# Optimization experiments

Measured on AMD Instinct MI355X. Metric: run time of the kernel, lower is better.

The kernel has to match this reference:

```python
import jax, jax.numpy as jnp
import numpy as np

D_MODEL, D_STATE, D_CONV, EXPAND = 1024, 16, 4, 2
D_INNER = D_MODEL * EXPAND


def setup_inputs() -> dict:
    key = jax.random.key(0)
    ks = jax.random.split(key, 12)
    s = lambda fan_in: 1.0 / np.sqrt(fan_in)
    return {
        "x": jax.random.normal(ks[0], (2, 2048, D_MODEL), dtype=jnp.float32),
        "W_in": jax.random.normal(ks[1], (D_MODEL, 2 * D_INNER), dtype=jnp.float32) * s(D_MODEL),
        "b_in": jnp.zeros((2 * D_INNER,), jnp.float32),
        "W_conv": jax.random.normal(ks[2], (D_INNER, 1, D_CONV), dtype=jnp.float32) * s(D_CONV),
        "b_conv": jnp.zeros((D_INNER,), jnp.float32),
        "A_log": jax.random.normal(ks[3], (D_INNER, D_STATE), dtype=jnp.float32) * -0.5 - 1.0,
        "D": jnp.ones((D_INNER,), jnp.float32),
        "W_B": jax.random.normal(ks[4], (D_INNER, D_STATE), dtype=jnp.float32) * s(D_INNER),
        "b_B": jnp.zeros((D_STATE,), jnp.float32),
        "W_C": jax.random.normal(ks[5], (D_INNER, D_STATE), dtype=jnp.float32) * s(D_INNER),
        "b_C": jnp.zeros((D_STATE,), jnp.float32),
        "W_out": jax.random.normal(ks[6], (D_INNER, D_MODEL), dtype=jnp.float32) * s(D_INNER),
        "b_out": jnp.zeros((D_MODEL,), jnp.float32),
    }


def reference(x, W_in, b_in, W_conv, b_conv, A_log, D, W_B, b_B, W_C, b_C, W_out, b_out):
    B, L, _ = x.shape
    xz = x @ W_in + b_in                       # (B, L, 2*D_INNER)
    xi, z = jnp.split(xz, 2, axis=-1)
    # depthwise causal conv1d (left pad d_conv-1, truncate to L)
    xc = jnp.swapaxes(xi, 1, 2)                # (B, D_INNER, L)
    xc = jax.lax.conv_general_dilated(
        xc, W_conv, window_strides=(1,), padding=[(D_CONV - 1, 0)],
        dimension_numbers=("NCH", "OIH", "NCH"), feature_group_count=D_INNER)
    xc = xc + b_conv[None, :, None]
    xi = jnp.swapaxes(xc, 1, 2)                # (B, L, D_INNER)
    xi = jax.nn.silu(xi)

    A = -jnp.exp(jnp.clip(A_log, -10.0, 2.0))  # (D_INNER, D_STATE)
    Bm = xi @ W_B + b_B                        # (B, L, D_STATE)
    Cm = xi @ W_C + b_C                        # (B, L, D_STATE)

    def step(h, inp):
        x_t, B_t, C_t = inp                    # (B,D_INNER), (B,D_STATE), (B,D_STATE)
        h = h * A[None] + x_t[:, :, None] * B_t[:, None, :]
        h = jnp.clip(h, -100.0, 100.0)
        y = jnp.einsum("bds,bs->bd", h, C_t) + D * x_t
        y = jnp.clip(y, -100.0, 100.0)
        return h, y

    h0 = jnp.zeros((B, D_INNER, D_STATE), x.dtype)
    xs = (jnp.swapaxes(xi, 0, 1), jnp.swapaxes(Bm, 0, 1), jnp.swapaxes(Cm, 0, 1))
    _, ys = jax.lax.scan(step, h0, xs)         # ys: (L, B, D_INNER)
    y = jnp.swapaxes(ys, 0, 1)                 # (B, L, D_INNER)
    y = y * jax.nn.sigmoid(z)
    return y @ W_out + b_out
```

## Files before the change

kernel.cpp:

```cpp
#include <hip/hip_runtime.h>
#include <hip/hip_bf16.h>
#include <math.h>

#define B_SZ   2
#define L_SZ   2048
#define DM     1024
#define DI     2048
#define DS     16
#define M_SZ   (B_SZ * L_SZ)
#define N_XZ   (2 * DI)
#define LDF    20
#define SEGS   32
#define SEGLEN 64
#define SEG1   32
#define KZN    8

typedef short bf16x8 __attribute__((ext_vector_type(8)));
typedef float f32x4  __attribute__((ext_vector_type(4)));

__device__ __forceinline__ unsigned short rne16(float f) {
  unsigned int u = __builtin_bit_cast(unsigned int, f);
  u += 0x7FFFu + ((u >> 16) & 1u);
  return (unsigned short)(u >> 16);
}
__device__ __forceinline__ float frombf(unsigned short h) {
  unsigned int u = ((unsigned int)h) << 16;
  return __builtin_bit_cast(float, u);
}

__global__ __launch_bounds__(256) void convert_x(
    const float* __restrict__ x, unsigned short* __restrict__ xh,
    unsigned short* __restrict__ xl) {
  int i = (blockIdx.x * 256 + threadIdx.x) * 4;
  float4 v = *(const float4*)(x + i);
  unsigned short h0 = rne16(v.x), h1 = rne16(v.y), h2 = rne16(v.z), h3 = rne16(v.w);
  *(ushort4*)(xh + i) = make_ushort4(h0, h1, h2, h3);
  *(ushort4*)(xl + i) = make_ushort4(rne16(v.x - frombf(h0)), rne16(v.y - frombf(h1)),
                                     rne16(v.z - frombf(h2)), rne16(v.w - frombf(h3)));
}

__global__ __launch_bounds__(256) void transpose_w(
    const float* __restrict__ in, int R, int C,
    unsigned short* __restrict__ oh, unsigned short* __restrict__ ol) {
  __shared__ float T[64][65];
  const int tid = threadIdx.x;
  const int c0 = blockIdx.x * 64, r0 = blockIdx.y * 64;
  const int cc = tid & 63, rq = tid >> 6;
  #pragma unroll
  for (int i = 0; i < 16; ++i) {
    int r = rq * 16 + i;
    T[r][cc] = in[(size_t)(r0 + r) * C + c0 + cc];
  }
  __syncthreads();
  #pragma unroll
  for (int i = 0; i < 16; ++i) {
    int c = rq * 16 + i;
    float v = T[cc][c];
    size_t o = (size_t)(c0 + c) * R + r0 + cc;
    unsigned short h = rne16(v);
    oh[o] = h;
    if (ol) ol[o] = rne16(v - frombf(h));
  }
}

template<int BN, bool X3, bool OUTBF16>
__global__ __launch_bounds__(256, X3 ? 3 : 4) void gemm_t(
    const unsigned short* __restrict__ Ah, const unsigned short* __restrict__ Al, int lda,
    const unsigned short* __restrict__ Bh, const unsigned short* __restrict__ Bl, int ldb,
    const float* __restrict__ bias, float* __restrict__ Cf,
    unsigned short* __restrict__ Cz, int ldc, int K) {
  constexpr int WN  = BN / 2;
  constexpr int FJ  = BN / 32;
  constexpr int BCH = BN / 64;
  __shared__ unsigned int AhS[128 * LDF];
  __shared__ unsigned int BhS[BN * LDF];
  __shared__ unsigned int AlS[X3 ? 128 * LDF : 4];
  __shared__ unsigned int BlS[X3 ? BN * LDF : 4];
  const int tid  = threadIdx.x;
  const int lane = tid & 63, wave = tid >> 6;
  const int wr = wave >> 1, wc = wave & 1;
  const int lm = lane & 15, lq = lane >> 4;
  const int row0 = blockIdx.y * 128, col0 = blockIdx.x * BN;

  f32x4 acc[4][FJ];
  #pragma unroll
  for (int i = 0; i < 4; ++i)
    #pragma unroll
    for (int j = 0; j < FJ; ++j) acc[i][j] = (f32x4){0.f, 0.f, 0.f, 0.f};

  for (int k0 = 0; k0 < K; k0 += 32) {
    __syncthreads();
    #pragma unroll
    for (int i = 0; i < 2; ++i) {
      int idx = tid + i * 256, r = idx >> 2, q = idx & 3;
      size_t go = (size_t)(row0 + r) * lda + k0 + q * 8;
      *(uint4*)&AhS[r * LDF + q * 4] = *(const uint4*)(Ah + go);
      if constexpr (X3)
        *(uint4*)&AlS[r * LDF + q * 4] = *(const uint4*)(Al + go);
    }
    #pragma unroll
    for (int i = 0; i < BCH; ++i) {
      int idx = tid + i * 256, r = idx >> 2, q = idx & 3;
      size_t go = (size_t)(col0 + r) * ldb + k0 + q * 8;
      *(uint4*)&BhS[r * LDF + q * 4] = *(const uint4*)(Bh + go);
      if constexpr (X3)
        *(uint4*)&BlS[r * LDF + q * 4] = *(const uint4*)(Bl + go);
    }
    __syncthreads();
    bf16x8 bh[FJ], bl[FJ];
    #pragma unroll
    for (int j = 0; j < FJ; ++j) {
      bh[j] = *(const bf16x8*)&BhS[(wc * WN + j * 16 + lm) * LDF + lq * 4];
      if constexpr (X3)
        bl[j] = *(const bf16x8*)&BlS[(wc * WN + j * 16 + lm) * LDF + lq * 4];
    }
    #pragma unroll
    for (int i = 0; i < 4; ++i) {
      bf16x8 ah = *(const bf16x8*)&AhS[(wr * 64 + i * 16 + lm) * LDF + lq * 4];
      bf16x8 al;
      if constexpr (X3)
        al = *(const bf16x8*)&AlS[(wr * 64 + i * 16 + lm) * LDF + lq * 4];
      #pragma unroll
      for (int j = 0; j < FJ; ++j) {
        acc[i][j] = __builtin_amdgcn_mfma_f32_16x16x32_bf16(ah, bh[j], acc[i][j], 0, 0, 0);
        if constexpr (X3) {
          acc[i][j] = __builtin_amdgcn_mfma_f32_16x16x32_bf16(ah, bl[j], acc[i][j], 0, 0, 0);
          acc[i][j] = __builtin_amdgcn_mfma_f32_16x16x32_bf16(al, bh[j], acc[i][j], 0, 0, 0);
        }
      }
    }
  }
  #pragma unroll
  for (int i = 0; i < 4; ++i) {
    #pragma unroll
    for (int j = 0; j < FJ; ++j) {
      int c = col0 + wc * WN + j * 16 + lm;
      float bs = bias[c];
      #pragma unroll
      for (int k = 0; k < 4; ++k) {
        int r = row0 + wr * 64 + i * 16 + lq * 4 + k;
        float v = acc[i][j][k] + bs;
        if constexpr (OUTBF16) Cz[(size_t)r * ldc + c] = rne16(v);
        else                   Cf[(size_t)r * ldc + c] = v;
      }
    }
  }
}

__global__ __launch_bounds__(256) void conv_silu_kernel(
    const float* __restrict__ xi, const float* __restrict__ Wc,
    const float* __restrict__ bc, float* __restrict__ xc) {
  int idx = blockIdx.x * blockDim.x + threadIdx.x;
  if (idx >= M_SZ * DI) return;
  int d  = idx & (DI - 1);
  int bl = idx >> 11;
  int l  = bl & (L_SZ - 1);
  float4 w = ((const float4*)Wc)[d];
  const float* base = xi + (size_t)bl * DI + d;
  float s = bc[d] + base[0] * w.w;
  if (l >= 1) s = fmaf(base[-DI],     w.z, s);
  if (l >= 2) s = fmaf(base[-2 * DI], w.y, s);
  if (l >= 3) s = fmaf(base[-3 * DI], w.x, s);
  float sig = 1.f / (1.f + expf(-s));
  xc[idx] = s * sig;
}

__global__ __launch_bounds__(256) void prep_wbc(
    const float* __restrict__ WB, const float* __restrict__ WC,
    unsigned short* __restrict__ Wh, unsigned short* __restrict__ Wl) {
  int idx = blockIdx.x * 256 + threadIdx.x;
  int c = idx >> 11, k = idx & 2047;
  float v = 0.f;
  if (c < 32) {
    const float* W = (c & 1) ? WC : WB;
    v = W[k * DS + (c >> 1)];
  }
  unsigned short h = rne16(v);
  Wh[idx] = h;
  Wl[idx] = rne16(v - frombf(h));
}

__global__ __launch_bounds__(256, 3) void gemm_bcf(
    const float* __restrict__ Af, int lda,
    const unsigned short* __restrict__ Bh, const unsigned short* __restrict__ Bl, int ldb,
    float* __restrict__ parts, int ldc, int Kslice) {
  __shared__ unsigned int AhS[128 * LDF];
  __shared__ unsigned int AlS[128 * LDF];
  __shared__ unsigned int BhS[64 * LDF];
  __shared__ unsigned int BlS[64 * LDF];
  const int tid  = threadIdx.x;
  const int lane = tid & 63, wave = tid >> 6;
  const int wr = wave >> 1, wc = wave & 1;
  const int lm = lane & 15, lq = lane >> 4;
  const int row0 = blockIdx.y * 128;
  const int kbase = blockIdx.x * Kslice;
  float* Cp = parts + (size_t)blockIdx.x * M_SZ * 64;

  f32x4 acc[4][2];
  #pragma unroll
  for (int i = 0; i < 4; ++i)
    #pragma unroll
    for (int j = 0; j < 2; ++j) acc[i][j] = (f32x4){0.f, 0.f, 0.f, 0.f};

  for (int k0 = kbase; k0 < kbase + Kslice; k0 += 32) {
    __syncthreads();
    #pragma unroll
    for (int i = 0; i < 4; ++i) {
      int idx = tid + i * 256, r = idx >> 3, q = idx & 7;
      float4 v = *(const float4*)(Af + (size_t)(row0 + r) * lda + k0 + q * 4);
      unsigned short h0 = rne16(v.x), h1 = rne16(v.y), h2 = rne16(v.z), h3 = rne16(v.w);
      AhS[r * LDF + q * 2]     = (unsigned)h0 | ((unsigned)h1 << 16);
      AhS[r * LDF + q * 2 + 1] = (unsigned)h2 | ((unsigned)h3 << 16);
      unsigned short l0 = rne16(v.x - frombf(h0)), l1 = rne16(v.y - frombf(h1));
      unsigned short l2 = rne16(v.z - frombf(h2)), l3 = rne16(v.w - frombf(h3));
      AlS[r * LDF + q * 2]     = (unsigned)l0 | ((unsigned)l1 << 16);
      AlS[r * LDF + q * 2 + 1] = (unsigned)l2 | ((unsigned)l3 << 16);
    }
    {
      int r = tid >> 2, q = tid & 3;
      size_t go = (size_t)r * ldb + k0 + q * 8;
      *(uint4*)&BhS[r * LDF + q * 4] = *(const uint4*)(Bh + go);
      *(uint4*)&BlS[r * LDF + q * 4] = *(const uint4*)(Bl + go);
    }
    __syncthreads();
    bf16x8 bh[2], bl[2];
    #pragma unroll
    for (int j = 0; j < 2; ++j) {
      bh[j] = *(const bf16x8*)&BhS[(wc * 32 + j * 16 + lm) * LDF + lq * 4];
      bl[j] = *(const bf16x8*)&BlS[(wc * 32 + j * 16 + lm) * LDF + lq * 4];
    }
    #pragma unroll
    for (int i = 0; i < 4; ++i) {
      bf16x8 ah = *(const bf16x8*)&AhS[(wr * 64 + i * 16 + lm) * LDF + lq * 4];
      bf16x8 al = *(const bf16x8*)&AlS[(wr * 64 + i * 16 + lm) * LDF + lq * 4];
      #pragma unroll
      for (int j = 0; j < 2; ++j) {
        acc[i][j] = __builtin_amdgcn_mfma_f32_16x16x32_bf16(ah, bh[j], acc[i][j], 0, 0, 0);
        acc[i][j] = __builtin_amdgcn_mfma_f32_16x16x32_bf16(ah, bl[j], acc[i][j], 0, 0, 0);
        acc[i][j] = __builtin_amdgcn_mfma_f32_16x16x32_bf16(al, bh[j], acc[i][j], 0, 0, 0);
      }
    }
  }
  #pragma unroll
  for (int i = 0; i < 4; ++i) {
    #pragma unroll
    for (int j = 0; j < 2; ++j) {
      int c = wc * 32 + j * 16 + lm;
      #pragma unroll
      for (int k = 0; k < 4; ++k) {
        int r = row0 + wr * 64 + i * 16 + lq * 4 + k;
        Cp[(size_t)r * ldc + c] = acc[i][j][k];
      }
    }
  }
}

__global__ __launch_bounds__(256) void prep_bc_sum(
    const float* __restrict__ parts,
    const float* __restrict__ bB, const float* __restrict__ bC,
    float* __restrict__ BCm2, float* __restrict__ Bp2) {
  int idx = blockIdx.x * 256 + threadIdx.x;
  int row = idx >> 5, c = idx & 31;
  float s = 0.f;
  #pragma unroll
  for (int kz = 0; kz < KZN; ++kz)
    s += parts[(size_t)kz * M_SZ * 64 + (size_t)row * 64 + c];
  s += (c & 1) ? bC[c >> 1] : bB[c >> 1];
  BCm2[(size_t)row * 64 + c] = s;
  if (!(c & 1))
    Bp2[(size_t)(row >> 1) * 32 + (c >> 1) * 2 + (row & 1)] = s;
}

__device__ __forceinline__ float clampA(float a) {
  return fminf(fmaxf(a, -10.f), 2.f);
}

__global__ __launch_bounds__(256, 1) void scan_pass1(
    const float* __restrict__ xc, const float* __restrict__ Bp2,
    const float* __restrict__ A_log, float* __restrict__ hseg) {
  const int b    = blockIdx.y;
  const int wave = threadIdx.x >> 6;
  const int lane = threadIdx.x & 63;
  const int dd   = lane >> 4, s = lane & 15;
  const int d    = blockIdx.x * 16 + wave * 4 + dd;

  const float A = -expf(clampA(A_log[d * DS + s]));
  float h = 0.f;

  const float* px = xc  + (size_t)b * L_SZ * DI + d;
  const float* pb = Bp2 + (size_t)b * (L_SZ / 2) * 32 + s * 2;

  float  x0[SEG1], x1[SEG1];
  float2 b0[SEG1 / 2], b1[SEG1 / 2];

  #pragma unroll
  for (int j = 0; j < SEG1; ++j) x0[j] = px[j * DI];
  #pragma unroll
  for (int j = 0; j < SEG1 / 2; ++j) b0[j] = *(const float2*)(pb + j * 32);
  px += SEG1 * DI; pb += (SEG1 / 2) * 32;

  for (int w = 0; w < 60; w += 2) {
    #pragma unroll
    for (int j = 0; j < SEG1; ++j) x1[j] = px[j * DI];
    #pragma unroll
    for (int j = 0; j < SEG1 / 2; ++j) b1[j] = *(const float2*)(pb + j * 32);
    px += SEG1 * DI; pb += (SEG1 / 2) * 32;
    #pragma unroll
    for (int j = 0; j < SEG1; ++j) {
      float bj = (j & 1) ? b0[j >> 1].y : b0[j >> 1].x;
      h = __builtin_amdgcn_fmed3f(fmaf(h, A, x0[j] * bj), -100.f, 100.f);
    }
    #pragma unroll
    for (int j = 0; j < SEG1; ++j) x0[j] = px[j * DI];
    #pragma unroll
    for (int j = 0; j < SEG1 / 2; ++j) b0[j] = *(const float2*)(pb + j * 32);
    px += SEG1 * DI; pb += (SEG1 / 2) * 32;
    #pragma unroll
    for (int j = 0; j < SEG1; ++j) {
      float bj = (j & 1) ? b1[j >> 1].y : b1[j >> 1].x;
      h = __builtin_amdgcn_fmed3f(fmaf(h, A, x1[j] * bj), -100.f, 100.f);
    }
    hseg[(((size_t)b * (SEGS - 1) + (w >> 1)) * DI + d) * DS + s] = h;
  }
  #pragma unroll
  for (int j = 0; j < SEG1; ++j) x1[j] = px[j * DI];
  #pragma unroll
  for (int j = 0; j < SEG1 / 2; ++j) b1[j] = *(const float2*)(pb + j * 32);
  #pragma unroll
  for (int j = 0; j < SEG1; ++j) {
    float bj = (j & 1) ? b0[j >> 1].y : b0[j >> 1].x;
    h = __builtin_amdgcn_fmed3f(fmaf(h, A, x0[j] * bj), -100.f, 100.f);
  }
  #pragma unroll
  for (int j = 0; j < SEG1; ++j) {
    float bj = (j & 1) ? b1[j >> 1].y : b1[j >> 1].x;
    h = __builtin_amdgcn_fmed3f(fmaf(h, A, x1[j] * bj), -100.f, 100.f);
  }
  hseg[(((size_t)b * (SEGS - 1) + 30) * DI + d) * DS + s] = h;
}

__global__ __launch_bounds__(256, 2) void scan_pass2(
    const float* __restrict__ xc, const float* __restrict__ BCm2,
    const unsigned short* __restrict__ zb,
    const float* __restrict__ A_log, const float* __restrict__ Dv,
    const float* __restrict__ hseg, unsigned short* __restrict__ yg) {
  const int b   = blockIdx.y >> 5;
  const int seg = blockIdx.y & 31;
  const int d   = blockIdx.x * 256 + threadIdx.x;

  float A[16], h[16];
  #pragma unroll
  for (int q = 0; q < 4; ++q) {
    float4 al = *(const float4*)(A_log + d * DS + q * 4);
    A[q * 4 + 0] = -expf(clampA(al.x));
    A[q * 4 + 1] = -expf(clampA(al.y));
    A[q * 4 + 2] = -expf(clampA(al.z));
    A[q * 4 + 3] = -expf(clampA(al.w));
  }
  const float Dr = Dv[d];
  if (seg == 0) {
    #pragma unroll
    for (int s = 0; s < 16; ++s) h[s] = 0.f;
  } else {
    const float* hp = hseg + (((size_t)b * (SEGS - 1) + seg - 1) * DI + d) * DS;
    #pragma unroll
    for (int q = 0; q < 4; ++q) {
      float4 hv = *(const float4*)(hp + q * 4);
      h[q * 4 + 0] = hv.x; h[q * 4 + 1] = hv.y;
      h[q * 4 + 2] = hv.z; h[q * 4 + 3] = hv.w;
    }
  }

  const int rbase = b * L_SZ + seg * SEGLEN;
  const float*          px  = xc  + (size_t)rbase * DI + d;
  const unsigned short* pz  = zb  + (size_t)rbase * DI + d;
  unsigned short*       py  = yg  + (size_t)rbase * DI + d;
  const float*          pbc = BCm2 + (size_t)rbase * 64;

  #pragma unroll 2
  for (int t = 0; t < SEGLEN; ++t) {
    const float x = px[t * DI];
    const float* bc = pbc + t * 64;
    float y = Dr * x;
    #pragma unroll
    for (int s = 0; s < 16; ++s) {
      h[s] = __builtin_amdgcn_fmed3f(fmaf(h[s], A[s], x * bc[s * 2]), -100.f, 100.f);
      y = fmaf(h[s], bc[s * 2 + 1], y);
    }
    y = __builtin_amdgcn_fmed3f(y, -100.f, 100.f);
    const float zf = frombf(pz[t * DI]);
    py[t * DI] = rne16(y * (1.f / (1.f + expf(-zf))));
  }
}

extern "C" void kernel_launch(void* const* d_in, const int* in_sizes, int n_in,
                              void* d_out, int out_size, void* d_ws, size_t ws_size,
                              hipStream_t stream) {
  const float* x      = (const float*)d_in[0];
  const float* W_in   = (const float*)d_in[1];
  const float* b_in   = (const float*)d_in[2];
  const float* W_conv = (const float*)d_in[3];
  const float* b_conv = (const float*)d_in[4];
  const float* A_log  = (const float*)d_in[5];
  const float* Dv     = (const float*)d_in[6];
  const float* W_B    = (const float*)d_in[7];
  const float* b_B    = (const float*)d_in[8];
  const float* W_C    = (const float*)d_in[9];
  const float* b_C    = (const float*)d_in[10];
  const float* W_out  = (const float*)d_in[11];
  const float* b_out  = (const float*)d_in[12];
  float* out = (float*)d_out;

  char* w = (char*)d_ws;
  float*          xi    = (float*)(w + 0);
  unsigned short* yg    = (unsigned short*)(w + 0);
  float*          parts = (float*)(w + 16777216);
  float*          hseg  = (float*)(w + 16777216);
  float*          BCm2  = (float*)(w + 25165824);
  float*          Bp2   = (float*)(w + 26214400);
  unsigned short* zb    = (unsigned short*)(w + 33554432);
  float*          xc    = (float*)(w + 50331648);
  unsigned short* xh    = (unsigned short*)(w + 50331648);
  unsigned short* xl    = (unsigned short*)(w + 58720256);
  unsigned short* WhT   = (unsigned short*)(w + 67108864);
  unsigned short* WlT   = (unsigned short*)(w + 75497472);
  unsigned short* WbcTh = (unsigned short*)(w + 83886080);
  unsigned short* WbcTl = (unsigned short*)(w + 84148224);
  unsigned short* WoT   = (unsigned short*)(w + 84410368);

  convert_x<<<M_SZ * DM / 1024, 256, 0, stream>>>(x, xh, xl);
  transpose_w<<<dim3(N_XZ / 64, DM / 64), 256, 0, stream>>>(W_in, DM, N_XZ, WhT, WlT);
  transpose_w<<<dim3(DM / 64, DI / 64), 256, 0, stream>>>(W_out, DI, DM, WoT, nullptr);
  prep_wbc<<<64 * 2048 / 256, 256, 0, stream>>>(W_B, W_C, WbcTh, WbcTl);

  gemm_t<128, true, false><<<dim3(DI / 128, M_SZ / 128), 256, 0, stream>>>(
      xh, xl, DM, WhT, WlT, DM, b_in, xi, nullptr, DI, DM);

  gemm_t<128, false, true><<<dim3(DI / 128, M_SZ / 128), 256, 0, stream>>>(
      xh, nullptr, DM, WhT + (size_t)DI * DM, nullptr, DM,
      b_in + DI, nullptr, zb, DI, DM);

  conv_silu_kernel<<<M_SZ * DI / 256, 256, 0, stream>>>(xi, W_conv, b_conv, xc);

  gemm_bcf<<<dim3(KZN, M_SZ / 128), 256, 0, stream>>>(
      xc, DI, WbcTh, WbcTl, DI, parts, 64, DI / KZN);
  prep_bc_sum<<<M_SZ * 32 / 256, 256, 0, stream>>>(parts, b_B, b_C, BCm2, Bp2);

  scan_pass1<<<dim3(DI / 16, B_SZ), 256, 0, stream>>>(xc, Bp2, A_log, hseg);

  scan_pass2<<<dim3(DI / 256, B_SZ * SEGS), 256, 0, stream>>>(
      xc, BCm2, zb, A_log, Dv, hseg, yg);

  gemm_t<64, false, false><<<dim3(DM / 64, M_SZ / 128), 256, 0, stream>>>(
      yg, nullptr, DI, WoT, nullptr, DI, b_out, out, nullptr, DM, DI);
}
```

Baseline: 393.1 us.

## Parallelize segment-carry scan via composed clamped affine maps per segment

Replaces the sequential pass-1 scan over all 2048 timesteps with a per-segment computation of the composed clamped-affine map (scale, offset, lower and upper clamp bounds). Each of the 32 segments runs in parallel, and a short serial combine over the segment maps then produces the segment-start states. The B coefficients are laid out time-contiguous per state so they can be read with float4 loads. This removes the long serial dependency chain and the low parallelism of the old pass 1. In exchange it does about four times more arithmetic per step, and the clamp composition has to match the original step-by-step clamping exactly.

```diff
diff --git a/kernel.cpp b/kernel.cpp
--- a/kernel.cpp
+++ b/kernel.cpp
@@ -12,7 +12,6 @@
 #define LDF    20
 #define SEGS   32
 #define SEGLEN 64
-#define SEG1   32
 #define KZN    8
 
 typedef short bf16x8 __attribute__((ext_vector_type(8)));
@@ -258,7 +257,7 @@
 __global__ __launch_bounds__(256) void prep_bc_sum(
     const float* __restrict__ parts,
     const float* __restrict__ bB, const float* __restrict__ bC,
-    float* __restrict__ BCm2, float* __restrict__ Bp2) {
+    float* __restrict__ BCm2, float* __restrict__ Bt) {
   int idx = blockIdx.x * 256 + threadIdx.x;
   int row = idx >> 5, c = idx & 31;
   float s = 0.f;
@@ -267,76 +266,76 @@
     s += parts[(size_t)kz * M_SZ * 64 + (size_t)row * 64 + c];
   s += (c & 1) ? bC[c >> 1] : bB[c >> 1];
   BCm2[(size_t)row * 64 + c] = s;
-  if (!(c & 1))
-    Bp2[(size_t)(row >> 1) * 32 + (c >> 1) * 2 + (row & 1)] = s;
+  if (!(c & 1)) {
+    int b = row >> 11, t = row & 2047;
+    Bt[((size_t)b * DS + (c >> 1)) * L_SZ + t] = s;
+  }
 }
 
 __device__ __forceinline__ float clampA(float a) {
   return fminf(fmaxf(a, -10.f), 2.f);
 }
 
-__global__ __launch_bounds__(256, 1) void scan_pass1(
-    const float* __restrict__ xc, const float* __restrict__ Bp2,
+#define LOADCH(xv, bv, base) { \
+  _Pragma("unroll") for (int j = 0; j < 16; ++j) xv[j] = px[(base + j) * DI]; \
+  _Pragma("unroll") for (int q = 0; q < 4; ++q) { \
+    float4 t4 = *(const float4*)(pB + base + q * 4); \
+    bv[q * 4] = t4.x; bv[q * 4 + 1] = t4.y; bv[q * 4 + 2] = t4.z; bv[q * 4 + 3] = t4.w; } }
+
+#define MSTEP(u) { \
+  float uu = (u); \
+  float nb = fmaf(A, bb, uu); \
+  float nl = __builtin_amdgcn_fmed3f(fmaf(A, hi, uu), -100.f, 100.f); \
+  float nh = __builtin_amdgcn_fmed3f(fmaf(A, lo, uu), -100.f, 100.f); \
+  a *= A; bb = nb; lo = nl; hi = nh; }
+
+__global__ __launch_bounds__(512, 1) void scan_maps(
+    const float* __restrict__ xc, const float* __restrict__ Bt,
     const float* __restrict__ A_log, float* __restrict__ hseg) {
-  const int b    = blockIdx.y;
-  const int wave = threadIdx.x >> 6;
-  const int lane = threadIdx.x & 63;
-  const int dd   = lane >> 4, s = lane & 15;
-  const int d    = blockIdx.x * 16 + wave * 4 + dd;
+  const int bid   = blockIdx.x;
+  const int chain = (bid & 7) * 512 + (bid >> 3);
+  const int b = chain >> 11, d = chain & 2047;
+  const int tid = threadIdx.x;
+  const int g = tid & 31;
+  const int s = tid >> 5;
 
   const float A = -expf(clampA(A_log[d * DS + s]));
-  float h = 0.f;
-
-  const float* px = xc  + (size_t)b * L_SZ * DI + d;
-  const float* pb = Bp2 + (size_t)b * (L_SZ / 2) * 32 + s * 2;
-
-  float  x0[SEG1], x1[SEG1];
-  float2 b0[SEG1 / 2], b1[SEG1 / 2];
-
-  #pragma unroll
-  for (int j = 0; j < SEG1; ++j) x0[j] = px[j * DI];
-  #pragma unroll
-  for (int j = 0; j < SEG1 / 2; ++j) b0[j] = *(const float2*)(pb + j * 32);
-  px += SEG1 * DI; pb += (SEG1 / 2) * 32;
-
-  for (int w = 0; w < 60; w += 2) {
-    #pragma unroll
-    for (int j = 0; j < SEG1; ++j) x1[j] = px[j * DI];
-    #pragma unroll
-    for (int j = 0; j < SEG1 / 2; ++j) b1[j] = *(const float2*)(pb + j * 32);
-    px += SEG1 * DI; pb += (SEG1 / 2) * 32;
-    #pragma unroll
-    for (int j = 0; j < SEG1; ++j) {
-      float bj = (j & 1) ? b0[j >> 1].y : b0[j >> 1].x;
-      h = __builtin_amdgcn_fmed3f(fmaf(h, A, x0[j] * bj), -100.f, 100.f);
-    }
-    #pragma unroll
-    for (int j = 0; j < SEG1; ++j) x0[j] = px[j * DI];
-    #pragma unroll
-    for (int j = 0; j < SEG1 / 2; ++j) b0[j] = *(const float2*)(pb + j * 32);
-    px += SEG1 * DI; pb += (SEG1 / 2) * 32;
-    #pragma unroll
-    for (int j = 0; j < SEG1; ++j) {
-      float bj = (j & 1) ? b1[j >> 1].y : b1[j >> 1].x;
-      h = __builtin_amdgcn_fmed3f(fmaf(h, A, x1[j] * bj), -100.f, 100.f);
-    }
-    hseg[(((size_t)b * (SEGS - 1) + (w >> 1)) * DI + d) * DS + s] = h;
-  }
-  #pragma unroll
-  for (int j = 0; j < SEG1; ++j) x1[j] = px[j * DI];
-  #pragma unroll
-  for (int j = 0; j < SEG1 / 2; ++j) b1[j] = *(const float2*)(pb + j * 32);
-  #pragma unroll
-  for (int j = 0; j < SEG1; ++j) {
-    float bj = (j & 1) ? b0[j >> 1].y : b0[j >> 1].x;
-    h = __builtin_amdgcn_fmed3f(fmaf(h, A, x0[j] * bj), -100.f, 100.f);
-  }
-  #pragma unroll
-  for (int j = 0; j < SEG1; ++j) {
-    float bj = (j & 1) ? b1[j >> 1].y : b1[j >> 1].x;
-    h = __builtin_amdgcn_fmed3f(fmaf(h, A, x1[j] * bj), -100.f, 100.f);
-  }
-  hseg[(((size_t)b * (SEGS - 1) + 30) * DI + d) * DS + s] = h;
+
+  const float* px = xc + ((size_t)b * L_SZ + g * SEGLEN) * DI + d;
+  const float* pB = Bt + ((size_t)b * DS + s) * L_SZ + g * SEGLEN;
+
+  float xa[16], ba[16], xn[16], bn[16];
+  LOADCH(xa, ba, 0)
+  LOADCH(xn, bn, 16)
+
+  float a = A, bb = xa[0] * ba[0], lo = -100.f, hi = 100.f;
+  #pragma unroll
+  for (int j = 1; j < 16; ++j) MSTEP(xa[j] * ba[j])
+  LOADCH(xa, ba, 32)
+  #pragma unroll
+  for (int j = 0; j < 16; ++j) MSTEP(xn[j] * bn[j])
+  LOADCH(xn, bn, 48)
+  #pragma unroll
+  for (int j = 0; j < 16; ++j) MSTEP(xa[j] * ba[j])
+  #pragma unroll
+  for (int j = 0; j < 16; ++j) MSTEP(xn[j] * bn[j])
+
+  a  = __builtin_amdgcn_fmed3f(a,  -1e30f, 1e30f);
+  bb = __builtin_amdgcn_fmed3f(bb, -1e30f, 1e30f);
+
+  __shared__ float LM[SEGS][DS][4];
+  LM[g][s][0] = a; LM[g][s][1] = bb; LM[g][s][2] = lo; LM[g][s][3] = hi;
+  __syncthreads();
+
+  if (tid < DS) {
+    float h = 0.f;
+    #pragma unroll
+    for (int k = 0; k < SEGS - 1; ++k) {
+      float4 m = *(const float4*)&LM[k][tid][0];
+      h = __builtin_amdgcn_fmed3f(fmaf(m.x, h, m.y), m.z, m.w);
+      hseg[(((size_t)b * (SEGS - 1) + k) * DI + d) * DS + tid] = h;
+    }
+  }
 }
 
 __global__ __launch_bounds__(256, 2) void scan_pass2(
@@ -417,7 +416,7 @@
   float*          parts = (float*)(w + 16777216);
   float*          hseg  = (float*)(w + 16777216);
   float*          BCm2  = (float*)(w + 25165824);
-  float*          Bp2   = (float*)(w + 26214400);
+  float*          Bt    = (float*)(w + 26214400);
   unsigned short* zb    = (unsigned short*)(w + 33554432);
   float*          xc    = (float*)(w + 50331648);
   unsigned short* xh    = (unsigned short*)(w + 50331648);
@@ -444,9 +443,9 @@
 
   gemm_bcf<<<dim3(KZN, M_SZ / 128), 256, 0, stream>>>(
       xc, DI, WbcTh, WbcTl, DI, parts, 64, DI / KZN);
-  prep_bc_sum<<<M_SZ * 32 / 256, 256, 0, stream>>>(parts, b_B, b_C, BCm2, Bp2);
-
-  scan_pass1<<<dim3(DI / 16, B_SZ), 256, 0, stream>>>(xc, Bp2, A_log, hseg);
+  prep_bc_sum<<<M_SZ * 32 / 256, 256, 0, stream>>>(parts, b_B, b_C, BCm2, Bt);
+
+  scan_maps<<<B_SZ * DI, 512, 0, stream>>>(xc, Bt, A_log, hseg);
 
   scan_pass2<<<dim3(DI / 256, B_SZ * SEGS), 256, 0, stream>>>(
       xc, BCm2, zb, A_log, Dv, hseg, yg);
```

Result: slower. 685.3 us (+74.3%).
